# Kernel optimization log

Hardware: AMD Instinct MI355X
Metric: run time of the kernel (lower is better)

The kernel has to match this reference:

```python
import jax, jax.numpy as jnp
import numpy as np

DEGREE = 3
NUM_VARS = 3
NUM_OUT = 3
BATCH, H, W = 16, 512, 512


def _generate_powers(order, n_variables):
    """Multivariate monomial exponent tuples, same order as the torch module."""
    pattern = [0] * n_variables
    yield tuple(pattern)
    for current_sum in range(1, order + 1):
        pattern[0] = current_sum
        yield tuple(pattern)
        while pattern[-1] < current_sum:
            for i in range(2, n_variables + 1):
                if 0 < pattern[n_variables - i]:
                    pattern[n_variables - i] -= 1
                    if 2 < i:
                        pattern[n_variables - i + 1] = 1 + pattern[-1]
                        pattern[-1] = 0
                    else:
                        pattern[-1] += 1
                    break
            yield tuple(pattern)
        pattern[-1] = 0


NUM_COEFFS = len(list(_generate_powers(DEGREE, NUM_VARS)))  # = C(6,3) = 20


def setup_inputs() -> dict:
    key = jax.random.key(0)
    k1, k2 = jax.random.split(key)
    img = jax.random.uniform(k1, (BATCH, NUM_VARS, H, W), dtype=jnp.float32)
    coeffs = jax.random.normal(k2, (BATCH, NUM_OUT, NUM_COEFFS), dtype=jnp.float32)
    # Non-trainable buffer holding monomial exponents, shape (num_coeffs, num_vars)
    powers = jnp.asarray(list(_generate_powers(DEGREE, NUM_VARS)), dtype=jnp.float32)
    return {"img": img, "coeffs": coeffs, "powers": powers}


def reference(img, coeffs, powers):
    # poly[b, c, x, y] = prod_v img[b, v, x, y] ** powers[c, v]
    # (matches torch: pow -> permute -> prod over variable dim)
    poly = jnp.prod(img[:, None, :, :, :] ** powers[None, :, :, None, None], axis=2)
    # out[b, o, x, y] = sum_c coeffs[b, o, c] * poly[b, c, x, y]
    return jnp.einsum('boc,bcxy->boxy', coeffs, poly)
```

## Files before the change

kernel.cpp:

```cpp
#include <hip/hip_runtime.h>


#define PLANE (512 * 512)
#define NC 20
#define NV 3
#define NO 3
#define NB 16

__device__ __forceinline__ int canon_idx(int a, int b, int c) {
    int d = a + b + c;
    if (d == 0) return 0;
    if (d == 1) return a ? 1 : (b ? 2 : 3);
    if (d == 2) {
        if (a == 2) return 4;
        if (a == 1) return (b == 1) ? 5 : 6;
        return (b == 2) ? 7 : ((b == 1) ? 8 : 9);
    }
    if (a == 3) return 10;
    if (a == 2) return (b == 1) ? 11 : 12;
    if (a == 1) return (b == 2) ? 13 : ((b == 1) ? 14 : 15);
    return (b == 3) ? 16 : ((b == 2) ? 17 : ((b == 1) ? 18 : 19));
}

__device__ __forceinline__ void eval_pixel(float x, float y, float z,
                                           const float (&cc)[NO * NC],
                                           float& o0, float& o1, float& o2) {
    float x2 = x * x, y2 = y * y, z2 = z * z;
    float xy = x * y, xz = x * z, yz = y * z;
    float m[NC];
    m[0] = 1.0f;    m[1] = x;       m[2] = y;       m[3] = z;
    m[4] = x2;      m[5] = xy;      m[6] = xz;      m[7] = y2;
    m[8] = yz;      m[9] = z2;      m[10] = x2 * x; m[11] = x2 * y;
    m[12] = x2 * z; m[13] = x * y2; m[14] = xy * z; m[15] = x * z2;
    m[16] = y2 * y; m[17] = y2 * z; m[18] = y * z2; m[19] = z2 * z;
    float a0 = 0.0f, a1 = 0.0f, a2 = 0.0f;
#pragma unroll
    for (int i = 0; i < NC; i++) {
        a0 = fmaf(cc[i],          m[i], a0);
        a1 = fmaf(cc[NC + i],     m[i], a1);
        a2 = fmaf(cc[2 * NC + i], m[i], a2);
    }
    o0 = a0; o1 = a1; o2 = a2;
}

__global__ __launch_bounds__(256) void channel_poly_kernel(
        const float* __restrict__ img,
        const float* __restrict__ coeffs,
        const float* __restrict__ powers,
        float* __restrict__ out) {
    const int b   = blockIdx.y;
    const int tid = threadIdx.x;

    __shared__ float cstage[NO * NC];
    if (tid < NO * NC) {
        int c  = tid % NC;
        int o  = tid / NC;
        int ea = (int)powers[c * NV + 0];
        int eb = (int)powers[c * NV + 1];
        int ec = (int)powers[c * NV + 2];
        cstage[o * NC + canon_idx(ea, eb, ec)] = coeffs[b * NO * NC + tid];
    }
    __syncthreads();

    float cc[NO * NC];
#pragma unroll
    for (int i = 0; i < NO * NC; i++) {
        cc[i] = __int_as_float(__builtin_amdgcn_readfirstlane(__float_as_int(cstage[i])));
    }

    const int t = blockIdx.x * blockDim.x + tid;

    const float* base = img + (size_t)b * NV * PLANE;
    const float4 X = ((const float4*)(base))[t];
    const float4 Y = ((const float4*)(base + PLANE))[t];
    const float4 Z = ((const float4*)(base + 2 * PLANE))[t];

    float4 O0, O1, O2;
    eval_pixel(X.x, Y.x, Z.x, cc, O0.x, O1.x, O2.x);
    eval_pixel(X.y, Y.y, Z.y, cc, O0.y, O1.y, O2.y);
    eval_pixel(X.z, Y.z, Z.z, cc, O0.z, O1.z, O2.z);
    eval_pixel(X.w, Y.w, Z.w, cc, O0.w, O1.w, O2.w);

    float* obase = out + (size_t)b * NO * PLANE;
    ((float4*)(obase))[t]             = O0;
    ((float4*)(obase + PLANE))[t]     = O1;
    ((float4*)(obase + 2 * PLANE))[t] = O2;
}

extern "C" void kernel_launch(void* const* d_in, const int* in_sizes, int n_in,
                              void* d_out, int out_size, void* d_ws, size_t ws_size,
                              hipStream_t stream) {
    const float* img    = (const float*)d_in[0];
    const float* coeffs = (const float*)d_in[1];
    const float* powers = (const float*)d_in[2];
    float* out = (float*)d_out;
    (void)d_ws; (void)ws_size;

    dim3 grid(PLANE / 4 / 256, NB);
    channel_poly_kernel<<<grid, dim3(256), 0, stream>>>(img, coeffs, powers, out);
}
```

Measured before the change: 102.6 us.

## Process four float4 groups per thread and prefetch inputs before coefficient setup

Each thread now handles four float4 pixel groups strided by the block width, and the grid shrinks accordingly. All image loads are issued before the shared-memory coefficient staging and barrier, so global load latency overlaps the per-block setup. The setup cost is spread over more pixels per block. Register use rises, which may reduce occupancy.

```diff
diff --git a/kernel.cpp b/kernel.cpp
--- a/kernel.cpp
+++ b/kernel.cpp
@@ -6,6 +6,7 @@
 #define NV 3
 #define NO 3
 #define NB 16
+#define G  4
 
 __device__ __forceinline__ int canon_idx(int a, int b, int c) {
     int d = a + b + c;
@@ -51,6 +52,20 @@
     const int b   = blockIdx.y;
     const int tid = threadIdx.x;
 
+    const int t0 = blockIdx.x * (256 * G) + tid;
+    const float* ibase = img + (size_t)b * NV * PLANE;
+    const float4* Xp = (const float4*)ibase;
+    const float4* Yp = (const float4*)(ibase + PLANE);
+    const float4* Zp = (const float4*)(ibase + 2 * PLANE);
+
+    float4 X[G], Y[G], Z[G];
+#pragma unroll
+    for (int g = 0; g < G; g++) {
+        X[g] = Xp[t0 + g * 256];
+        Y[g] = Yp[t0 + g * 256];
+        Z[g] = Zp[t0 + g * 256];
+    }
+
     __shared__ float cstage[NO * NC];
     if (tid < NO * NC) {
         int c  = tid % NC;
@@ -68,23 +83,22 @@
         cc[i] = __int_as_float(__builtin_amdgcn_readfirstlane(__float_as_int(cstage[i])));
     }
 
-    const int t = blockIdx.x * blockDim.x + tid;
+    float* obase = out + (size_t)b * NO * PLANE;
+    float4* O0p = (float4*)obase;
+    float4* O1p = (float4*)(obase + PLANE);
+    float4* O2p = (float4*)(obase + 2 * PLANE);
 
-    const float* base = img + (size_t)b * NV * PLANE;
-    const float4 X = ((const float4*)(base))[t];
-    const float4 Y = ((const float4*)(base + PLANE))[t];
-    const float4 Z = ((const float4*)(base + 2 * PLANE))[t];
-
-    float4 O0, O1, O2;
-    eval_pixel(X.x, Y.x, Z.x, cc, O0.x, O1.x, O2.x);
-    eval_pixel(X.y, Y.y, Z.y, cc, O0.y, O1.y, O2.y);
-    eval_pixel(X.z, Y.z, Z.z, cc, O0.z, O1.z, O2.z);
-    eval_pixel(X.w, Y.w, Z.w, cc, O0.w, O1.w, O2.w);
-
-    float* obase = out + (size_t)b * NO * PLANE;
-    ((float4*)(obase))[t]             = O0;
-    ((float4*)(obase + PLANE))[t]     = O1;
-    ((float4*)(obase + 2 * PLANE))[t] = O2;
+#pragma unroll
+    for (int g = 0; g < G; g++) {
+        float4 O0, O1, O2;
+        eval_pixel(X[g].x, Y[g].x, Z[g].x, cc, O0.x, O1.x, O2.x);
+        eval_pixel(X[g].y, Y[g].y, Z[g].y, cc, O0.y, O1.y, O2.y);
+        eval_pixel(X[g].z, Y[g].z, Z[g].z, cc, O0.z, O1.z, O2.z);
+        eval_pixel(X[g].w, Y[g].w, Z[g].w, cc, O0.w, O1.w, O2.w);
+        O0p[t0 + g * 256] = O0;
+        O1p[t0 + g * 256] = O1;
+        O2p[t0 + g * 256] = O2;
+    }
 }
 
 extern "C" void kernel_launch(void* const* d_in, const int* in_sizes, int n_in,
@@ -96,6 +110,6 @@
     float* out = (float*)d_out;
     (void)d_ws; (void)ws_size;
 
-    dim3 grid(PLANE / 4 / 256, NB);
+    dim3 grid(PLANE / 4 / 256 / G, NB);
     channel_poly_kernel<<<grid, dim3(256), 0, stream>>>(img, coeffs, powers, out);
 }
```

Measured after the change: 101.4 us. About the same (-1.1%).
